# Performance work log

Measured on AMD Instinct MI355X. Metric: run time of the kernel, lower is better.

## Reference

```python
import jax, jax.numpy as jnp
import numpy as np

N, E, D, R = 100000, 640000, 128, 4


def setup_inputs() -> dict:
    key = jax.random.key(0)
    ks = jax.random.split(key, 5)
    x = jax.random.normal(ks[0], (N, D), dtype=jnp.float32)
    edge_index = jax.random.randint(ks[1], (2, E), 0, N, dtype=jnp.int64)
    edge_attr = jax.random.randint(ks[2], (E,), 0, R, dtype=jnp.int64)
    # Per-relation GraphConv weights (conv_layer instantiated as PyG GraphConv, aggr='add')
    W_rel = jax.random.normal(ks[3], (R, D, D), dtype=jnp.float32) / np.sqrt(D).astype(np.float32)
    b_rel = jnp.zeros((R, D), dtype=jnp.float32)
    W_root = jax.random.normal(ks[4], (R, D, D), dtype=jnp.float32) / np.sqrt(D).astype(np.float32)
    b_root = jnp.zeros((R, D), dtype=jnp.float32)
    return {"x": x, "edge_index": edge_index, "edge_attr": edge_attr,
            "W_rel": W_rel, "b_rel": b_rel, "W_root": W_root, "b_root": b_root}


def reference(x, edge_index, edge_attr, W_rel, b_rel, W_root, b_root):
    # Fused equivalent of: sum_r tanh(GraphConv_r(x, edge_index[:, edge_attr==r]))
    # GraphConv_r(x, ei) = segment_sum(x[src], dst) @ W_rel[r] + b_rel[r] + x @ W_root[r] + b_root[r]
    src, dst = edge_index[0], edge_index[1]
    msgs = x[src]                                  # [E, D] single gather for all relations
    seg = dst * R + edge_attr                      # combined (node, relation) segment id
    agg = jax.ops.segment_sum(msgs, seg, num_segments=N * R).reshape(N, R, D)
    rel = jnp.einsum('nrd,rde->nre', agg, W_rel) + b_rel    # [N, R, D]
    root = jnp.einsum('nd,rde->nre', x, W_root) + b_root    # [N, R, D]
    return jnp.tanh(rel + root).sum(axis=1)       # accumulate over relations -> [N, D]
```

## Files before the change

kernel.cpp:

```cpp
#include <hip/hip_runtime.h>
#include <stdint.h>

#define D 128
#define RNUM 4
#define TM 32
#define CAP 16
#define LSTRIDE 272
#define GEMM_BLOCKS 512

typedef unsigned short u16;
typedef __attribute__((ext_vector_type(8))) short short8;
typedef __attribute__((ext_vector_type(4))) float floatx4;

__device__ inline u16 f2bf(float f) {
  union { float f; uint32_t u; } c; c.f = f;
  uint32_t r = (c.u + 0x7FFFu + ((c.u >> 16) & 1u)) >> 16;
  return (u16)r;
}
__device__ inline uint32_t pack2(float a, float b) {
  return (uint32_t)f2bf(a) | ((uint32_t)f2bf(b) << 16);
}
__device__ inline float bflo(uint32_t w) {
  union { uint32_t u; float f; } c; c.u = w << 16; return c.f;
}
__device__ inline float bfhi(uint32_t w) {
  union { uint32_t u; float f; } c; c.u = w & 0xFFFF0000u; return c.f;
}

__device__ inline float fast_tanh(float v) {
  float a = fabsf(v);
  float e = __builtin_amdgcn_exp2f(a * 2.8853900817779268f);
  float t = 1.0f - 2.0f * __builtin_amdgcn_rcpf(e + 1.0f);
  return copysignf(t, v);
}

__global__ void prep_kernel(const float* __restrict__ x,
                            const float* __restrict__ W_rel, const float* __restrict__ b_rel,
                            const float* __restrict__ W_root, const float* __restrict__ b_root,
                            u16* __restrict__ Wt, float* __restrict__ bias,
                            u16* __restrict__ x16, uint32_t* __restrict__ cursor,
                            int total8, int nseg) {
  int idx = blockIdx.x * 256 + threadIdx.x;
  if (idx < total8) {
    const float4* s = (const float4*)(x + (size_t)idx * 8);
    float4 lo = s[0], hi = s[1];
    uint4 pk;
    pk.x = pack2(lo.x, lo.y); pk.y = pack2(lo.z, lo.w);
    pk.z = pack2(hi.x, hi.y); pk.w = pack2(hi.z, hi.w);
    *(uint4*)(x16 + (size_t)idx * 8) = pk;
  }
  if (idx < nseg) cursor[idx] = 0u;
  if (idx < RNUM * D) bias[idx] = b_rel[idx] + b_root[idx];
  if (idx < RNUM * D * 2 * D) {
    int k   = idx & 255;
    int col = (idx >> 8) & 127;
    int r   = idx >> 15;
    float v = (k < D) ? W_rel[((size_t)r * D + k) * D + col]
                      : W_root[((size_t)r * D + (k - D)) * D + col];
    Wt[idx] = f2bf(v);
  }
}

__global__ void bin_kernel(const int* __restrict__ ei, const int* __restrict__ ea,
                           uint32_t* __restrict__ cursor, uint32_t* __restrict__ bins, int E) {
  int t = blockIdx.x * 256 + threadIdx.x;
  if (t >= E) return;
  uint32_t seg = (uint32_t)ei[E + t] * 4u + (uint32_t)ea[t];
  uint32_t pos = atomicAdd(&cursor[seg], 1u);
  if (pos < (uint32_t)CAP) bins[(size_t)seg * CAP + pos] = (uint32_t)ei[t];
}

__global__ __launch_bounds__(256, 8) void gather_kernel(
    const u16* __restrict__ x16, const uint32_t* __restrict__ bins,
    const uint32_t* __restrict__ cursor, u16* __restrict__ agg16, int nseg) {
  __shared__ __align__(16) uint32_t sList[4 * LSTRIDE];

  const int tid = threadIdx.x;
  const int w = tid >> 6, l = tid & 63;
  const uint32_t segBase = (uint32_t)blockIdx.x * 64 + (uint32_t)w * 16;

  {
    uint4 z4 = {0u, 0u, 0u, 0u};
    uint4* zl = (uint4*)sList;
#pragma unroll
    for (int i = 0; i < 2; ++i) {
      int idx = tid + i * 256;
      if (idx < 4 * LSTRIDE / 4) zl[idx] = z4;
    }
  }
  __syncthreads();

  uint32_t cnt = 0;
  if (l < 16 && segBase + l < (uint32_t)nseg) {
    uint32_t c = cursor[segBase + l];
    cnt = c < (uint32_t)CAP ? c : (uint32_t)CAP;
  }
  uint32_t run = cnt;
#pragma unroll
  for (int dlt = 1; dlt < 16; dlt <<= 1) {
    int v = __shfl_up((int)run, dlt, 16);
    if ((l & 15) >= dlt) run += (uint32_t)v;
  }
  uint32_t offx = run - cnt;
  uint32_t total = (uint32_t)__builtin_amdgcn_readfirstlane(__shfl((int)run, 15));

  uint32_t* wl = &sList[w * LSTRIDE];
  {
    int row = l >> 2, sb = (l & 3) * 4;
    uint32_t rowcnt = (uint32_t)__shfl((int)cnt, row);
    uint32_t rowoff = (uint32_t)__shfl((int)offx, row);
    uint4 rc4 = *(const uint4*)(bins + (size_t)(segBase + row) * CAP + sb);
    uint32_t tag = (uint32_t)row << 20;
    if ((uint32_t)(sb + 0) < rowcnt) wl[rowoff + sb + 0] = (rc4.x & 0x1FFFFu) | tag;
    if ((uint32_t)(sb + 1) < rowcnt) wl[rowoff + sb + 1] = (rc4.y & 0x1FFFFu) | tag;
    if ((uint32_t)(sb + 2) < rowcnt) wl[rowoff + sb + 2] = (rc4.z & 0x1FFFFu) | tag;
    if ((uint32_t)(sb + 3) < rowcnt) wl[rowoff + sb + 3] = (rc4.w & 0x1FFFFu) | tag;
  }
  __asm volatile("s_waitcnt lgkmcnt(0)");

  int curRow = -1;
  uint32_t written = 0;
  float ax = 0.f, ay = 0.f;
  for (uint32_t i = 0; i < total; i += 8) {
    uint4 ra = *(const uint4*)&wl[i];
    uint4 rb = *(const uint4*)&wl[i + 4];
    uint32_t r8[8] = {ra.x, ra.y, ra.z, ra.w, rb.x, rb.y, rb.z, rb.w};
    uint32_t wv[8];
#pragma unroll
    for (int j = 0; j < 8; ++j)
      wv[j] = *(const uint32_t*)(x16 + (size_t)(r8[j] & 0x1FFFFu) * D + 2 * l);
#pragma unroll
    for (int j = 0; j < 8; ++j) {
      if (i + (uint32_t)j < total) {
        int rj = (int)(r8[j] >> 20);
        if (rj != curRow) {
          if (curRow >= 0) {
            *(uint32_t*)(agg16 + (size_t)(segBase + curRow) * D + 2 * l) = pack2(ax, ay);
            written |= 1u << curRow;
          }
          ax = 0.f; ay = 0.f; curRow = rj;
        }
        ax += bflo(wv[j]); ay += bfhi(wv[j]);
      }
    }
  }
  if (curRow >= 0) {
    *(uint32_t*)(agg16 + (size_t)(segBase + curRow) * D + 2 * l) = pack2(ax, ay);
    written |= 1u << curRow;
  }
  for (int t = 0; t < 16; ++t) {
    if (!(written & (1u << t)) && segBase + t < (uint32_t)nseg)
      *(uint32_t*)(agg16 + (size_t)(segBase + t) * D + 2 * l) = 0u;
  }
}

__global__ __launch_bounds__(512, 2) void gemm_kernel(
    const u16* __restrict__ agg16, const u16* __restrict__ x16,
    const u16* __restrict__ Wt, const float* __restrict__ bias,
    float* __restrict__ out, int N, int tiles, int tpb) {
  __shared__ __align__(16) u16 sA[5 * TM * D];

  const int tid = threadIdx.x;
  const int w = tid >> 6, l = tid & 63;
  const int lrow = l & 15, lhi = l >> 4;
  const int col = w * 16 + lrow;

  short8 breg[RNUM][8];
  float bb[RNUM];
#pragma unroll
  for (int r = 0; r < RNUM; ++r) {
    bb[r] = bias[r * D + col];
#pragma unroll
    for (int ks = 0; ks < 8; ++ks)
      breg[r][ks] = *(const short8*)(Wt + ((size_t)(r * D + col) * (2 * D) + ks * 32 + lhi * 8));
  }

  const int t0 = blockIdx.x * tpb;
  const int t1 = (t0 + tpb < tiles) ? (t0 + tpb) : tiles;
  if (t0 >= tiles) return;

  const int sc = tid & 15, snode = tid >> 4;
  uint4 stage[5];

  auto issue = [&](int tile) {
    int gnode = tile * TM + snode;
#pragma unroll
    for (int k = 0; k < 5; ++k) {
      uint4 pk = {0u, 0u, 0u, 0u};
      if (gnode < N) {
        const u16* src = (k < 4) ? (agg16 + ((size_t)gnode * 4 + k) * D + sc * 8)
                                 : (x16 + (size_t)gnode * D + sc * 8);
        pk = *(const uint4*)src;
      }
      stage[k] = pk;
    }
  };
  auto commit = [&]() {
#pragma unroll
    for (int k = 0; k < 5; ++k)
      *(uint4*)&sA[k * (TM * D) + snode * D + ((sc ^ (snode & 7)) << 3)] = stage[k];
  };

  issue(t0);
  commit();
  if (t0 + 1 < t1) issue(t0 + 1);
  __syncthreads();

  for (int t = t0; t < t1; ++t) {
    floatx4 oacc[2];
    oacc[0] = (floatx4){0.f, 0.f, 0.f, 0.f};
    oacc[1] = (floatx4){0.f, 0.f, 0.f, 0.f};

#pragma unroll
    for (int r = 0; r < RNUM; ++r) {
      floatx4 acc[2];
      acc[0] = (floatx4){0.f, 0.f, 0.f, 0.f};
      acc[1] = (floatx4){0.f, 0.f, 0.f, 0.f};
#pragma unroll
      for (int ks = 0; ks < 8; ++ks) {
        const u16* Abase = (ks < 4) ? (sA + r * (TM * D)) : (sA + 4 * (TM * D));
        const int cRead = (ks & 3) * 4 + lhi;
#pragma unroll
        for (int m = 0; m < 2; ++m) {
          int node = m * 16 + lrow;
          short8 afr = *(const short8*)&Abase[node * D + ((cRead ^ (node & 7)) << 3)];
          acc[m] = __builtin_amdgcn_mfma_f32_16x16x32_bf16(afr, breg[r][ks], acc[m], 0, 0, 0);
        }
      }
#pragma unroll
      for (int m = 0; m < 2; ++m)
#pragma unroll
        for (int j = 0; j < 4; ++j)
          oacc[m][j] += fast_tanh(acc[m][j] + bb[r]);
    }

    const int nodeBase = t * TM;
#pragma unroll
    for (int m = 0; m < 2; ++m) {
#pragma unroll
      for (int j = 0; j < 4; ++j) {
        int node = nodeBase + m * 16 + lhi * 4 + j;
        if (node < N) out[(size_t)node * D + col] = oacc[m][j];
      }
    }

    __syncthreads();
    if (t + 1 < t1) {
      commit();
      issue(t + 2);
    }
    __syncthreads();
  }
}

extern "C" void kernel_launch(void* const* d_in, const int* in_sizes, int n_in,
                              void* d_out, int out_size, void* d_ws, size_t ws_size,
                              hipStream_t stream) {
  const float* x      = (const float*)d_in[0];
  const int*   ei     = (const int*)d_in[1];
  const int*   ea     = (const int*)d_in[2];
  const float* W_rel  = (const float*)d_in[3];
  const float* b_rel  = (const float*)d_in[4];
  const float* W_root = (const float*)d_in[5];
  const float* b_root = (const float*)d_in[6];
  float* out = (float*)d_out;

  const int N = in_sizes[0] / D;
  const int E = in_sizes[2];
  const int NB = (N + TM - 1) / TM;
  const int NSEG = N * RNUM;
  const int total8 = N * (D / 8);
  const int GB = (NSEG + 63) / 64;
  const int tpb = (NB + GEMM_BLOCKS - 1) / GEMM_BLOCKS;

  size_t o = 0;
  auto nxt = [&](size_t bytes) { size_t p = o; o += (bytes + 255) & ~(size_t)255; return p; };
  u16*      Wt     = (u16*)((char*)d_ws + nxt((size_t)RNUM * D * 2 * D * 2));
  float*    bias   = (float*)((char*)d_ws + nxt((size_t)RNUM * D * 4));
  uint32_t* cursor = (uint32_t*)((char*)d_ws + nxt((size_t)NSEG * 4));
  uint32_t* bins   = (uint32_t*)((char*)d_ws + nxt((size_t)NSEG * CAP * 4));
  u16*      x16    = (u16*)((char*)d_ws + nxt((size_t)N * D * 2));
  u16*      agg16  = (u16*)((char*)d_ws + nxt((size_t)NSEG * D * 2));

  prep_kernel<<<(total8 + 255) / 256, 256, 0, stream>>>(x, W_rel, b_rel, W_root, b_root,
                                                        Wt, bias, x16, cursor, total8, NSEG);
  bin_kernel<<<(E + 255) / 256, 256, 0, stream>>>(ei, ea, cursor, bins, E);
  gather_kernel<<<GB, 256, 0, stream>>>(x16, bins, cursor, agg16, NSEG);
  gemm_kernel<<<GEMM_BLOCKS, 512, 0, stream>>>(agg16, x16, Wt, bias, out, N, NB, tpb);
}
```

Baseline: 156.8 us.

## Split relations across wave halves in GEMM with LDS reduction and balanced tiles

The GEMM kernel now launches 1024-thread blocks, and each half of the waves handles two of the four relations. This halves the weight-register footprint per wave. The two halves' tanh sums are combined through a padded LDS buffer before the output store. Tile staging is spread over all 1024 threads, and tiles are divided evenly across 256 blocks instead of by ceiling division. The cost is extra LDS traffic and a reduction step on every tile.

```diff
diff --git a/kernel.cpp b/kernel.cpp
--- a/kernel.cpp
+++ b/kernel.cpp
@@ -6,7 +6,7 @@
 #define TM 32
 #define CAP 16
 #define LSTRIDE 272
-#define GEMM_BLOCKS 512
+#define GEMM_BLOCKS 256
 
 typedef unsigned short u16;
 typedef __attribute__((ext_vector_type(8))) short short8;
@@ -154,51 +154,65 @@
   }
 }
 
-__global__ __launch_bounds__(512, 2) void gemm_kernel(
+__global__ __launch_bounds__(1024, 4) void gemm_kernel(
     const u16* __restrict__ agg16, const u16* __restrict__ x16,
     const u16* __restrict__ Wt, const float* __restrict__ bias,
-    float* __restrict__ out, int N, int tiles, int tpb) {
+    float* __restrict__ out, int N, int tiles) {
   __shared__ __align__(16) u16 sA[5 * TM * D];
+  __shared__ __align__(16) float red[8 * TM * 17];
 
   const int tid = threadIdx.x;
   const int w = tid >> 6, l = tid & 63;
+  const int g = w & 7, h = w >> 3;
   const int lrow = l & 15, lhi = l >> 4;
-  const int col = w * 16 + lrow;
-
-  short8 breg[RNUM][8];
-  float bb[RNUM];
-#pragma unroll
-  for (int r = 0; r < RNUM; ++r) {
-    bb[r] = bias[r * D + col];
+  const int col = g * 16 + lrow;
+
+  short8 breg[2][8];
+  float bb[2];
+#pragma unroll
+  for (int rr = 0; rr < 2; ++rr) {
+    int r = 2 * h + rr;
+    bb[rr] = bias[r * D + col];
 #pragma unroll
     for (int ks = 0; ks < 8; ++ks)
-      breg[r][ks] = *(const short8*)(Wt + ((size_t)(r * D + col) * (2 * D) + ks * 32 + lhi * 8));
-  }
-
-  const int t0 = blockIdx.x * tpb;
-  const int t1 = (t0 + tpb < tiles) ? (t0 + tpb) : tiles;
-  if (t0 >= tiles) return;
-
-  const int sc = tid & 15, snode = tid >> 4;
-  uint4 stage[5];
-
+      breg[rr][ks] = *(const short8*)(Wt + ((size_t)(r * D + col) * (2 * D) + ks * 32 + lhi * 8));
+  }
+
+  const int bid = blockIdx.x;
+  const int base = tiles / GEMM_BLOCKS, rem = tiles % GEMM_BLOCKS;
+  const int t0 = bid * base + (bid < rem ? bid : rem);
+  const int t1 = t0 + base + (bid < rem ? 1 : 0);
+  if (t0 >= t1) return;
+
+  uint4 stage[3];
   auto issue = [&](int tile) {
-    int gnode = tile * TM + snode;
-#pragma unroll
-    for (int k = 0; k < 5; ++k) {
-      uint4 pk = {0u, 0u, 0u, 0u};
-      if (gnode < N) {
-        const u16* src = (k < 4) ? (agg16 + ((size_t)gnode * 4 + k) * D + sc * 8)
-                                 : (x16 + (size_t)gnode * D + sc * 8);
-        pk = *(const uint4*)src;
+#pragma unroll
+    for (int k = 0; k < 3; ++k) {
+      int id = tid + k * 1024;
+      if (id < 2560) {
+        int slot = id >> 9, within = id & 511;
+        int c = within & 15, node = within >> 4;
+        int gnode = tile * TM + node;
+        uint4 pk = {0u, 0u, 0u, 0u};
+        if (gnode < N) {
+          const u16* src = (slot < 4) ? (agg16 + ((size_t)gnode * 4 + slot) * D + c * 8)
+                                      : (x16 + (size_t)gnode * D + c * 8);
+          pk = *(const uint4*)src;
+        }
+        stage[k] = pk;
       }
-      stage[k] = pk;
     }
   };
   auto commit = [&]() {
 #pragma unroll
-    for (int k = 0; k < 5; ++k)
-      *(uint4*)&sA[k * (TM * D) + snode * D + ((sc ^ (snode & 7)) << 3)] = stage[k];
+    for (int k = 0; k < 3; ++k) {
+      int id = tid + k * 1024;
+      if (id < 2560) {
+        int slot = id >> 9, within = id & 511;
+        int c = within & 15, node = within >> 4;
+        *(uint4*)&sA[slot * (TM * D) + node * D + ((c ^ (node & 7)) << 3)] = stage[k];
+      }
+    }
   };
 
   issue(t0);
@@ -212,7 +226,8 @@
     oacc[1] = (floatx4){0.f, 0.f, 0.f, 0.f};
 
 #pragma unroll
-    for (int r = 0; r < RNUM; ++r) {
+    for (int rr = 0; rr < 2; ++rr) {
+      const int r = 2 * h + rr;
       floatx4 acc[2];
       acc[0] = (floatx4){0.f, 0.f, 0.f, 0.f};
       acc[1] = (floatx4){0.f, 0.f, 0.f, 0.f};
@@ -224,30 +239,43 @@
         for (int m = 0; m < 2; ++m) {
           int node = m * 16 + lrow;
           short8 afr = *(const short8*)&Abase[node * D + ((cRead ^ (node & 7)) << 3)];
-          acc[m] = __builtin_amdgcn_mfma_f32_16x16x32_bf16(afr, breg[r][ks], acc[m], 0, 0, 0);
+          acc[m] = __builtin_amdgcn_mfma_f32_16x16x32_bf16(afr, breg[rr][ks], acc[m], 0, 0, 0);
         }
       }
 #pragma unroll
       for (int m = 0; m < 2; ++m)
 #pragma unroll
         for (int j = 0; j < 4; ++j)
-          oacc[m][j] += fast_tanh(acc[m][j] + bb[r]);
-    }
-
-    const int nodeBase = t * TM;
-#pragma unroll
-    for (int m = 0; m < 2; ++m) {
-#pragma unroll
-      for (int j = 0; j < 4; ++j) {
-        int node = nodeBase + m * 16 + lhi * 4 + j;
-        if (node < N) out[(size_t)node * D + col] = oacc[m][j];
-      }
-    }
-
+          oacc[m][j] += fast_tanh(acc[m][j] + bb[rr]);
+    }
+
+    if (h == 0) {
+#pragma unroll
+      for (int m = 0; m < 2; ++m)
+#pragma unroll
+        for (int j = 0; j < 4; ++j) {
+          int row = m * 16 + lhi * 4 + j;
+          red[g * (TM * 17) + row * 17 + lrow] = oacc[m][j];
+        }
+    }
     __syncthreads();
+
     if (t + 1 < t1) {
       commit();
       issue(t + 2);
+    }
+
+    if (h == 1) {
+      const int nodeBase = t * TM;
+#pragma unroll
+      for (int m = 0; m < 2; ++m)
+#pragma unroll
+        for (int j = 0; j < 4; ++j) {
+          int row = m * 16 + lhi * 4 + j;
+          int node = nodeBase + row;
+          if (node < N)
+            out[(size_t)node * D + col] = oacc[m][j] + red[g * (TM * 17) + row * 17 + lrow];
+        }
     }
     __syncthreads();
   }
@@ -271,7 +299,6 @@
   const int NSEG = N * RNUM;
   const int total8 = N * (D / 8);
   const int GB = (NSEG + 63) / 64;
-  const int tpb = (NB + GEMM_BLOCKS - 1) / GEMM_BLOCKS;
 
   size_t o = 0;
   auto nxt = [&](size_t bytes) { size_t p = o; o += (bytes + 255) & ~(size_t)255; return p; };
@@ -286,5 +313,5 @@
                                                         Wt, bias, x16, cursor, total8, NSEG);
   bin_kernel<<<(E + 255) / 256, 256, 0, stream>>>(ei, ea, cursor, bins, E);
   gather_kernel<<<GB, 256, 0, stream>>>(x16, bins, cursor, agg16, NSEG);
-  gemm_kernel<<<GEMM_BLOCKS, 512, 0, stream>>>(agg16, x16, Wt, bias, out, N, NB, tpb);
-}
+  gemm_kernel<<<GEMM_BLOCKS, 1024, 0, stream>>>(agg16, x16, Wt, bias, out, N, NB);
+}
```

Result: slower. 201.2 us (+28.4%).
